# Optimization experiments

Measured on AMD Instinct MI355X. Metric: run time of the kernel, lower is better.

## Reference

```python
import jax, jax.numpy as jnp
import numpy as np

B, S, D, H = 32, 8192, 128, 256  # batch-of-MLPs, seq_len, emb_dim, hidden_dim
LN_EPS = 1e-5


def setup_inputs() -> dict:
    key = jax.random.key(0)
    k0, k1, k2, k3 = jax.random.split(key, 4)
    x = jax.random.normal(k0, (B, S, D), dtype=jnp.float32)
    # shared learned Q projection (torch Linear stores W as [out,in]; y = x @ W.T)
    Wq = jax.random.normal(k1, (D, D), dtype=jnp.float32) / np.float32(np.sqrt(D))
    # per-batch-index (non-shared) fast-weight MLP params
    W1 = jax.random.normal(k2, (B, D, H), dtype=jnp.float32) / np.float32(np.sqrt(D))
    b1 = jnp.zeros((B, H), dtype=jnp.float32)
    W2 = jax.random.normal(k3, (B, H, D), dtype=jnp.float32) / np.float32(np.sqrt(H))
    b2 = jnp.zeros((B, D), dtype=jnp.float32)
    gamma = jnp.ones((B, D), dtype=jnp.float32)
    beta = jnp.zeros((B, D), dtype=jnp.float32)
    return dict(x=x, Wq=Wq, W1=W1, b1=b1, W2=W2, b2=b2, gamma=gamma, beta=beta)


def reference(x, Wq, W1, b1, W2, b2, gamma, beta):
    # queries = silu(Q(x))
    q = jax.nn.silu(jnp.einsum('bsd,ed->bse', x, Wq))
    # torch F.normalize with default dim=1 -> L2-normalize over the sequence axis
    q = q / jnp.clip(jnp.linalg.norm(q, axis=1, keepdims=True), 1e-12)
    # ParallelMLPs: per-index MLP with distinct weights (grouped GEMM), + residual
    h = jax.nn.silu(jnp.einsum('bsd,bdh->bsh', q, W1) + b1[:, None, :])
    o = jnp.einsum('bsh,bhd->bsd', h, W2) + b2[:, None, :]
    mu = jnp.mean(o, axis=-1, keepdims=True)
    var = jnp.mean(jnp.square(o - mu), axis=-1, keepdims=True)
    ln = (o - mu) / jnp.sqrt(var + LN_EPS) * gamma[:, None, :] + beta[:, None, :]
    return ln + q
```

## Files before the change

### kernel.cpp

```cpp
#include <hip/hip_runtime.h>
#include <stdint.h>

#define B_ 32
#define S_ 8192
#define D_ 128
#define H_ 256

typedef __attribute__((ext_vector_type(4))) float f32x4;
typedef __attribute__((ext_vector_type(8))) short bf16x8;
typedef __attribute__((ext_vector_type(4))) unsigned int u32x4;

__device__ __forceinline__ unsigned short f2bf(float f) {
    union { float f; unsigned int u; } v; v.f = f;
    unsigned int r = v.u + 0x7fffu + ((v.u >> 16) & 1u);
    return (unsigned short)(r >> 16);
}
__device__ __forceinline__ float bf2f(unsigned short u) {
    union { unsigned int u; float f; } v; v.u = ((unsigned int)u) << 16;
    return v.f;
}
__device__ __forceinline__ float silu_f(float v) {
    return v / (1.0f + __expf(-v));
}
__device__ __forceinline__ unsigned int cvtpk(float lo, float hi) {
    unsigned int r;
    asm("v_cvt_pk_bf16_f32 %0, %1, %2" : "=v"(r) : "v"(lo), "v"(hi));
    return r;
}
__device__ __forceinline__ void gl16(const void* g, void* l) {
    __builtin_amdgcn_global_load_lds(
        (const __attribute__((address_space(1))) unsigned int*)g,
        (__attribute__((address_space(3))) unsigned int*)l, 16, 0, 0);
}

__global__ void k_prep(const float* __restrict__ Wq, const float* __restrict__ W1,
                       const float* __restrict__ W2,
                       unsigned short* __restrict__ wq_bf,
                       unsigned short* __restrict__ w1t,
                       unsigned short* __restrict__ w2s) {
    __shared__ __align__(16) unsigned short tile[64 * 64];
    int t = threadIdx.x, blk = blockIdx.x;
    if (blk < 512) {
        int b = blk >> 4, ht = (blk >> 2) & 3, dt = blk & 3;
        int h0 = ht * 64, d0 = dt * 32;
#pragma unroll
        for (int i = 0; i < 2; i++) {
            int idx = t + i * 256;
            int h = idx >> 3, d4 = (idx & 7) * 4;
            f32x4 v = *(const f32x4*)(W2 + ((size_t)(b * H_ + h0 + h)) * D_ + d0 + d4);
#pragma unroll
            for (int j = 0; j < 4; j++) tile[(d4 + j) * 64 + h] = f2bf(v[j]);
        }
        __syncthreads();
        int r = t >> 3, c = t & 7;
        int d = d0 + r;
        u32x4 v = *(const u32x4*)(tile + r * 64 + c * 8);
        *(u32x4*)((char*)w2s + (size_t)(b * 4 + ht) * 16384 + d * 128 + ((c ^ (d & 7)) << 4)) = v;
    } else if (blk < 768) {
        int a = blk - 512;
        int b = a >> 3, dt = (a >> 2) & 1, ht = a & 3;
        int d0 = dt * 64, h0 = ht * 64;
#pragma unroll
        for (int i = 0; i < 4; i++) {
            int idx = t + i * 256;
            int d = idx >> 4, h4 = (idx & 15) * 4;
            f32x4 v = *(const f32x4*)(W1 + ((size_t)(b * D_ + d0 + d)) * H_ + h0 + h4);
#pragma unroll
            for (int j = 0; j < 4; j++) tile[(h4 + j) * 64 + d] = f2bf(v[j]);
        }
        __syncthreads();
#pragma unroll
        for (int i = 0; i < 2; i++) {
            int idx = t + i * 256;
            int h = idx >> 3, c = idx & 7;
            u32x4 v = *(const u32x4*)(tile + h * 64 + c * 8);
            *(u32x4*)(w1t + ((size_t)(b * H_ + h0 + h)) * D_ + d0 + c * 8) = v;
        }
    } else {
        int i = (blk - 768) * 256 + t;
        wq_bf[i] = f2bf(Wq[i]);
    }
}

__global__ __launch_bounds__(256, 2) void k_qproj(
        const float* __restrict__ x, const unsigned short* __restrict__ wq_bf,
        unsigned short* __restrict__ q_ws, float* __restrict__ part) {
    __shared__ __align__(16) unsigned short lds_a[128 * 128];
    __shared__ __align__(16) unsigned short lds_b[128 * 128];
    __shared__ float lds_ss[4][128];

    int tid = threadIdx.x;
    int lane = tid & 63, w = tid >> 6;
    int g = lane >> 4, c15 = lane & 15;
    int blk = blockIdx.x;
    int b = blk >> 6, st = blk & 63;
    size_t rowbase = (size_t)b * S_ + (size_t)st * 128;
    const float* xg = x + rowbase * D_;

    char* pA = (char*)lds_a;
    char* pB = (char*)lds_b;

#pragma unroll
    for (int i = 0; i < 8; i++) {
        int idx = tid + i * 256;
        int row = idx >> 4, cb = idx & 15;
        u32x4 v = *(const u32x4*)(wq_bf + row * 128 + cb * 8);
        *(u32x4*)(pB + row * 256 + (((unsigned)cb ^ (unsigned)(row & 7)) << 4)) = v;
    }
#pragma unroll
    for (int i = 0; i < 16; i++) {
        int idx = tid + i * 256;
        int row = idx >> 5, c4 = idx & 31;
        f32x4 v = *(const f32x4*)(xg + (size_t)row * 128 + c4 * 4);
        union { unsigned short s[4]; unsigned long long u; } o;
        o.s[0] = f2bf(v[0]); o.s[1] = f2bf(v[1]); o.s[2] = f2bf(v[2]); o.s[3] = f2bf(v[3]);
        *(unsigned long long*)(pA + row * 256 + ((c4 * 8) ^ ((row & 7) << 4))) = o.u;
    }
    __syncthreads();

    f32x4 acc[2][8];
#pragma unroll
    for (int m = 0; m < 2; m++)
#pragma unroll
        for (int n = 0; n < 8; n++) acc[m][n] = (f32x4)0.0f;

#pragma unroll
    for (int kk = 0; kk < 4; kk++) {
        int kb = kk * 64 + (g << 4);
        bf16x8 a[2];
#pragma unroll
        for (int m = 0; m < 2; m++) {
            int row = (w << 5) + (m << 4) + c15;
            a[m] = *(const bf16x8*)(pA + row * 256 + (kb ^ ((row & 7) << 4)));
        }
#pragma unroll
        for (int n = 0; n < 8; n++) {
            int rowb = (n << 4) + c15;
            bf16x8 bb = *(const bf16x8*)(pB + rowb * 256 + (kb ^ ((rowb & 7) << 4)));
#pragma unroll
            for (int m = 0; m < 2; m++)
                acc[m][n] = __builtin_amdgcn_mfma_f32_16x16x32_bf16(a[m], bb, acc[m][n], 0, 0, 0);
        }
    }

    float ss[8];
#pragma unroll
    for (int n = 0; n < 8; n++) ss[n] = 0.0f;
#pragma unroll
    for (int m = 0; m < 2; m++)
#pragma unroll
        for (int n = 0; n < 8; n++)
#pragma unroll
            for (int r = 0; r < 4; r++) {
                float v = silu_f(acc[m][n][r]);
                acc[m][n][r] = v;
                ss[n] += v * v;
            }
#pragma unroll
    for (int n = 0; n < 8; n++) {
        float v = ss[n];
        v += __shfl_xor(v, 16, 64);
        v += __shfl_xor(v, 32, 64);
        if (lane < 16) lds_ss[w][(n << 4) + lane] = v;
    }
    __syncthreads();

#pragma unroll
    for (int m = 0; m < 2; m++)
#pragma unroll
        for (int n = 0; n < 8; n++)
#pragma unroll
            for (int r = 0; r < 4; r++) {
                int row = (w << 5) + (m << 4) + (g << 2) + r;
                int col = (n << 4) + c15;
                int byte = row * 256 + (((col >> 3) ^ (row & 7)) << 4) + ((col & 7) * 2);
                *(unsigned short*)(pA + byte) = f2bf(acc[m][n][r]);
            }
    __syncthreads();

    char* qimg = (char*)q_ws + (size_t)(b * 64 + st) * 32768;
#pragma unroll
    for (int i = 0; i < 8; i++) {
        int off = tid * 16 + i * 4096;
        *(u32x4*)(qimg + off) = *(const u32x4*)(pA + off);
    }
    if (tid < 128) {
        float s = lds_ss[0][tid] + lds_ss[1][tid] + lds_ss[2][tid] + lds_ss[3][tid];
        part[((size_t)b * 64 + st) * 128 + tid] = s;
    }
}

__global__ void k_scale(const float* __restrict__ part, float* __restrict__ scale) {
    int idx = blockIdx.x * 256 + threadIdx.x;
    int b = idx >> 7, e = idx & 127;
    const float* p = part + (size_t)b * 64 * 128 + e;
    float s = 0.0f;
    for (int t = 0; t < 64; t++) s += p[t * 128];
    scale[idx] = 1.0f / fmaxf(sqrtf(s), 1e-12f);
}

__global__ void k_wscale(unsigned short* __restrict__ w1t, const float* __restrict__ scale) {
    int blk = blockIdx.x;
    int b = blk >> 2;
    char* region = (char*)w1t + (size_t)blk * 16384;
    int t = threadIdx.x;
    u32x4 v[4]; int hh[4], cc[4];
#pragma unroll
    for (int i = 0; i < 4; i++) {
        int cid = t + i * 256;
        hh[i] = cid >> 4; cc[i] = cid & 15;
        v[i] = *(const u32x4*)(region + hh[i] * 256 + cc[i] * 16);
    }
    __syncthreads();
#pragma unroll
    for (int i = 0; i < 4; i++) {
        union { unsigned short s[8]; u32x4 u; } o;
        const unsigned short* pv = (const unsigned short*)&v[i];
        const float* sc = scale + b * D_ + cc[i] * 8;
#pragma unroll
        for (int j = 0; j < 8; j++) o.s[j] = f2bf(bf2f(pv[j]) * sc[j]);
        *(u32x4*)(region + hh[i] * 256 + ((cc[i] ^ (hh[i] & 7)) << 4)) = o.u;
    }
}

__global__ __launch_bounds__(256, 2) void k_mlp(
        const unsigned short* __restrict__ q_img, const float* __restrict__ scale,
        const unsigned short* __restrict__ w1s, const unsigned short* __restrict__ w2s,
        const float* __restrict__ b1, const float* __restrict__ b2,
        const float* __restrict__ gamma, const float* __restrict__ beta,
        float* __restrict__ out) {
    __shared__ __align__(16) char lds[81920];
    int tid = threadIdx.x;
    int lane = tid & 63, w = tid >> 6;
    int g = lane >> 4, c15 = lane & 15;
    int blk = blockIdx.x;
    int b = blk >> 6, st = blk & 63;

    const char* qimg = (const char*)q_img + (size_t)(b * 64 + st) * 32768;
    const char* w1img = (const char*)w1s + (size_t)(b * 4) * 16384;
    const char* w2img = (const char*)w2s + (size_t)(b * 4) * 16384;

#pragma unroll
    for (int i = 0; i < 8; i++) {
        int off = w * 1024 + i * 4096;
        gl16(qimg + off + lane * 16, lds + off);
    }
#pragma unroll
    for (int i = 0; i < 4; i++) {
        int off = w * 1024 + i * 4096;
        gl16(w1img + off + lane * 16, lds + 32768 + off);
        gl16(w2img + off + lane * 16, lds + 49152 + off);
    }
    __syncthreads();

    f32x4 acco[2][8];
#pragma unroll
    for (int sm = 0; sm < 2; sm++)
#pragma unroll
        for (int dn = 0; dn < 8; dn++) acco[sm][dn] = (f32x4)0.0f;

#pragma unroll 1
    for (int hc = 0; hc < 4; hc++) {
        f32x4 b1v[4];
#pragma unroll
        for (int n = 0; n < 4; n++)
            b1v[n] = *(const f32x4*)(b1 + b * H_ + hc * 64 + n * 16 + g * 4);

        f32x4 acch[2][4];
#pragma unroll
        for (int sm = 0; sm < 2; sm++)
#pragma unroll
            for (int n = 0; n < 4; n++) acch[sm][n] = (f32x4)0.0f;
#pragma unroll
        for (int kk = 0; kk < 4; kk++) {
            bf16x8 qf[2];
#pragma unroll
            for (int sm = 0; sm < 2; sm++) {
                int row = w * 32 + sm * 16 + c15;
                qf[sm] = *(const bf16x8*)(lds + row * 256 + (((kk * 4 + g) ^ (row & 7)) << 4));
            }
#pragma unroll
            for (int n = 0; n < 4; n++) {
                int row = n * 16 + c15;
                bf16x8 wf = *(const bf16x8*)(lds + 32768 + row * 256 + (((kk * 4 + g) ^ (row & 7)) << 4));
#pragma unroll
                for (int sm = 0; sm < 2; sm++)
                    acch[sm][n] = __builtin_amdgcn_mfma_f32_16x16x32_bf16(wf, qf[sm], acch[sm][n], 0, 0, 0);
            }
        }

#pragma unroll
        for (int sm = 0; sm < 2; sm++) {
            int rl = sm * 16 + c15;
#pragma unroll
            for (int n = 0; n < 4; n++) {
                float v0 = silu_f(acch[sm][n][0] + b1v[n][0]);
                float v1 = silu_f(acch[sm][n][1] + b1v[n][1]);
                float v2 = silu_f(acch[sm][n][2] + b1v[n][2]);
                float v3 = silu_f(acch[sm][n][3] + b1v[n][3]);
                unsigned int lo = cvtpk(v0, v1), hi = cvtpk(v2, v3);
                int byte = 65536 + w * 4096 + rl * 128 + ((n * 32 + g * 8) ^ ((rl & 7) << 4));
                *(unsigned long long*)(lds + byte) =
                    ((unsigned long long)hi << 32) | (unsigned long long)lo;
            }
        }

#pragma unroll
        for (int kt = 0; kt < 2; kt++) {
            bf16x8 ha[2];
#pragma unroll
            for (int sm = 0; sm < 2; sm++) {
                int rl = sm * 16 + c15;
                ha[sm] = *(const bf16x8*)(lds + 65536 + w * 4096 + rl * 128 +
                                          ((kt * 64 + g * 16) ^ ((rl & 7) << 4)));
            }
#pragma unroll
            for (int dn = 0; dn < 8; dn++) {
                int row = dn * 16 + c15;
                bf16x8 wf = *(const bf16x8*)(lds + 49152 + row * 128 + (((kt * 4 + g) ^ (row & 7)) << 4));
#pragma unroll
                for (int sm = 0; sm < 2; sm++)
                    acco[sm][dn] = __builtin_amdgcn_mfma_f32_16x16x32_bf16(ha[sm], wf, acco[sm][dn], 0, 0, 0);
            }
        }

        if (hc < 3) {
            __syncthreads();
#pragma unroll
            for (int i = 0; i < 4; i++) {
                int off = w * 1024 + i * 4096;
                gl16(w1img + (hc + 1) * 16384 + off + lane * 16, lds + 32768 + off);
                gl16(w2img + (hc + 1) * 16384 + off + lane * 16, lds + 49152 + off);
            }
            __syncthreads();
        }
    }

    float scv[8], gv[8], bev[8], b2v[8];
#pragma unroll
    for (int dn = 0; dn < 8; dn++) {
        int col = dn * 16 + c15;
        scv[dn] = scale[b * 128 + col];
        gv[dn] = gamma[b * 128 + col];
        bev[dn] = beta[b * 128 + col];
        b2v[dn] = b2[b * 128 + col];
    }
    float* og = out + ((size_t)b * S_ + (size_t)st * 128) * D_;
#pragma unroll
    for (int sm = 0; sm < 2; sm++) {
#pragma unroll
        for (int r = 0; r < 4; r++) {
            int row = w * 32 + sm * 16 + g * 4 + r;
            float v[8];
            float s = 0.0f, s2 = 0.0f;
#pragma unroll
            for (int dn = 0; dn < 8; dn++) {
                v[dn] = acco[sm][dn][r] + b2v[dn];
                s += v[dn]; s2 += v[dn] * v[dn];
            }
            s += __shfl_xor(s, 1, 64);  s2 += __shfl_xor(s2, 1, 64);
            s += __shfl_xor(s, 2, 64);  s2 += __shfl_xor(s2, 2, 64);
            s += __shfl_xor(s, 4, 64);  s2 += __shfl_xor(s2, 4, 64);
            s += __shfl_xor(s, 8, 64);  s2 += __shfl_xor(s2, 8, 64);
            float mu = s * (1.0f / 128.0f);
            float var = s2 * (1.0f / 128.0f) - mu * mu;
            float rstd = rsqrtf(var + 1e-5f);
#pragma unroll
            for (int dn = 0; dn < 8; dn++) {
                int col = dn * 16 + c15;
                int byte = row * 256 + (((col >> 3) ^ (row & 7)) << 4) + ((col & 7) * 2);
                float qv = bf2f(*(const unsigned short*)(lds + byte)) * scv[dn];
                og[(size_t)row * 128 + col] = (v[dn] - mu) * rstd * gv[dn] + bev[dn] + qv;
            }
        }
    }
}

extern "C" void kernel_launch(void* const* d_in, const int* in_sizes, int n_in,
                              void* d_out, int out_size, void* d_ws, size_t ws_size,
                              hipStream_t stream) {
    (void)in_sizes; (void)n_in; (void)out_size; (void)ws_size;
    const float* x     = (const float*)d_in[0];
    const float* Wq    = (const float*)d_in[1];
    const float* W1    = (const float*)d_in[2];
    const float* b1    = (const float*)d_in[3];
    const float* W2    = (const float*)d_in[4];
    const float* b2    = (const float*)d_in[5];
    const float* gamma = (const float*)d_in[6];
    const float* beta  = (const float*)d_in[7];
    float* out = (float*)d_out;

    char* ws = (char*)d_ws;
    unsigned short* wq_bf = (unsigned short*)(ws);
    unsigned short* w1t   = (unsigned short*)(ws + 32768);
    unsigned short* w2s   = (unsigned short*)(ws + 32768 + 2097152);
    float* part           = (float*)(ws + 32768 + 2 * 2097152);
    float* scale          = (float*)(ws + 32768 + 2 * 2097152 + 1048576);
    unsigned short* q_ws  = (unsigned short*)(ws + 32768 + 2 * 2097152 + 1048576 + 16384);

    hipLaunchKernelGGL(k_prep, dim3(832), dim3(256), 0, stream, Wq, W1, W2, wq_bf, w1t, w2s);
    hipLaunchKernelGGL(k_qproj, dim3(2048), dim3(256), 0, stream, x, wq_bf, q_ws, part);
    hipLaunchKernelGGL(k_scale, dim3(16), dim3(256), 0, stream, part, scale);
    hipLaunchKernelGGL(k_wscale, dim3(128), dim3(256), 0, stream, w1t, scale);
    hipLaunchKernelGGL(k_mlp, dim3(2048), dim3(256), 0, stream,
                       q_ws, scale, w1t, w2s, b1, b2, gamma, beta, out);
}
```

Before: 147.4 us.

## Switch MLP to 32x32x16 MFMA with register-resident hidden activations and double buffering

Rewrites the fused MLP kernel to use 32x32x16 bf16 MFMA tiles. Q fragments are held in registers, and the SiLU hidden activations are passed straight into the second GEMM via permlane32 swaps instead of a round trip through LDS. The weight, bias and q images are pre-laid out in MFMA fragment order, and the W1/W2 chunks are double-buffered so the next chunk loads while the current one computes, removing one barrier pair per chunk. The cost is more register pressure and a more intricate fragment layout that must match across the prep, qproj and mlp kernels.

```diff
diff --git a/kernel.cpp b/kernel.cpp
--- a/kernel.cpp
+++ b/kernel.cpp
@@ -7,6 +7,7 @@
 #define H_ 256
 
 typedef __attribute__((ext_vector_type(4))) float f32x4;
+typedef __attribute__((ext_vector_type(16))) float f32x16;
 typedef __attribute__((ext_vector_type(8))) short bf16x8;
 typedef __attribute__((ext_vector_type(4))) unsigned int u32x4;
 
@@ -27,6 +28,9 @@
     asm("v_cvt_pk_bf16_f32 %0, %1, %2" : "=v"(r) : "v"(lo), "v"(hi));
     return r;
 }
+__device__ __forceinline__ void plswap(unsigned int& a, unsigned int& b) {
+    asm("v_permlane32_swap_b32 %0, %1" : "+v"(a), "+v"(b));
+}
 __device__ __forceinline__ void gl16(const void* g, void* l) {
     __builtin_amdgcn_global_load_lds(
         (const __attribute__((address_space(1))) unsigned int*)g,
@@ -34,57 +38,67 @@
 }
 
 __global__ void k_prep(const float* __restrict__ Wq, const float* __restrict__ W1,
-                       const float* __restrict__ W2,
+                       const float* __restrict__ W2, const float* __restrict__ b1,
                        unsigned short* __restrict__ wq_bf,
-                       unsigned short* __restrict__ w1t,
-                       unsigned short* __restrict__ w2s) {
-    __shared__ __align__(16) unsigned short tile[64 * 64];
+                       unsigned short* __restrict__ w1s,
+                       unsigned short* __restrict__ w2s,
+                       float* __restrict__ b1r) {
+    __shared__ __align__(16) unsigned short tile[8192];
     int t = threadIdx.x, blk = blockIdx.x;
-    if (blk < 512) {
-        int b = blk >> 4, ht = (blk >> 2) & 3, dt = blk & 3;
-        int h0 = ht * 64, d0 = dt * 32;
-#pragma unroll
-        for (int i = 0; i < 2; i++) {
+    if (blk < 128) {
+        int b = blk >> 2, hc = blk & 3;
+#pragma unroll
+        for (int i = 0; i < 8; i++) {
             int idx = t + i * 256;
-            int h = idx >> 3, d4 = (idx & 7) * 4;
-            f32x4 v = *(const f32x4*)(W2 + ((size_t)(b * H_ + h0 + h)) * D_ + d0 + d4);
-#pragma unroll
-            for (int j = 0; j < 4; j++) tile[(d4 + j) * 64 + h] = f2bf(v[j]);
+            int d = idx >> 4, hj = idx & 15;
+            f32x4 v = *(const f32x4*)(W1 + ((size_t)(b * D_ + d)) * H_ + hc * 64 + hj * 4);
+#pragma unroll
+            for (int u = 0; u < 4; u++) tile[(hj * 4 + u) * 128 + d] = f2bf(v[u]);
         }
         __syncthreads();
-        int r = t >> 3, c = t & 7;
-        int d = d0 + r;
-        u32x4 v = *(const u32x4*)(tile + r * 64 + c * 8);
-        *(u32x4*)((char*)w2s + (size_t)(b * 4 + ht) * 16384 + d * 128 + ((c ^ (d & 7)) << 4)) = v;
-    } else if (blk < 768) {
-        int a = blk - 512;
-        int b = a >> 3, dt = (a >> 2) & 1, ht = a & 3;
-        int d0 = dt * 64, h0 = ht * 64;
+        char* img = (char*)w1s + (size_t)blk * 16384;
 #pragma unroll
         for (int i = 0; i < 4; i++) {
+            int c = t + i * 256;
+            int n = c >> 9, kk = (c >> 6) & 7, l = c & 63;
+            u32x4 v = *(const u32x4*)(tile + (n * 32 + (l & 31)) * 128 + kk * 16 + (l >> 5) * 8);
+            *(u32x4*)(img + c * 16) = v;
+        }
+    } else if (blk < 256) {
+        int a = blk - 128;
+        int b = a >> 2, hc = a & 3;
+#pragma unroll
+        for (int i = 0; i < 8; i++) {
             int idx = t + i * 256;
-            int d = idx >> 4, h4 = (idx & 15) * 4;
-            f32x4 v = *(const f32x4*)(W1 + ((size_t)(b * D_ + d0 + d)) * H_ + h0 + h4);
-#pragma unroll
-            for (int j = 0; j < 4; j++) tile[(h4 + j) * 64 + d] = f2bf(v[j]);
+            int h = idx >> 5, d4 = idx & 31;
+            f32x4 v = *(const f32x4*)(W2 + ((size_t)(b * H_ + hc * 64 + h)) * D_ + d4 * 4);
+#pragma unroll
+            for (int u = 0; u < 4; u++) tile[(d4 * 4 + u) * 64 + h] = f2bf(v[u]);
         }
         __syncthreads();
-#pragma unroll
-        for (int i = 0; i < 2; i++) {
-            int idx = t + i * 256;
-            int h = idx >> 3, c = idx & 7;
-            u32x4 v = *(const u32x4*)(tile + h * 64 + c * 8);
-            *(u32x4*)(w1t + ((size_t)(b * H_ + h0 + h)) * D_ + d0 + c * 8) = v;
-        }
+        char* img = (char*)w2s + (size_t)a * 16384;
+#pragma unroll
+        for (int i = 0; i < 4; i++) {
+            int c = t + i * 256;
+            int dn = c >> 8, n = (c >> 7) & 1, kk2 = (c >> 6) & 1, l = c & 63;
+            u32x4 v = *(const u32x4*)(tile + (dn * 32 + (l & 31)) * 64 + n * 32 + kk2 * 16 + (l >> 5) * 8);
+            *(u32x4*)(img + c * 16) = v;
+        }
+    } else if (blk < 320) {
+        int i = (blk - 256) * 256 + t;
+        wq_bf[i] = f2bf(Wq[i]);
     } else {
-        int i = (blk - 768) * 256 + t;
-        wq_bf[i] = f2bf(Wq[i]);
+        int idx = (blk - 320) * 256 + t;
+        int b = idx >> 8, rem = idx & 255;
+        int hc = rem >> 6, n = (rem >> 5) & 1, hi = (rem >> 4) & 1, r = rem & 15;
+        int h = hc * 64 + n * 32 + (r & 3) + 8 * (r >> 2) + 4 * hi;
+        b1r[idx] = b1[b * H_ + h];
     }
 }
 
 __global__ __launch_bounds__(256, 2) void k_qproj(
         const float* __restrict__ x, const unsigned short* __restrict__ wq_bf,
-        unsigned short* __restrict__ q_ws, float* __restrict__ part) {
+        unsigned short* __restrict__ q_img, float* __restrict__ part) {
     __shared__ __align__(16) unsigned short lds_a[128 * 128];
     __shared__ __align__(16) unsigned short lds_b[128 * 128];
     __shared__ float lds_ss[4][128];
@@ -112,9 +126,9 @@
         int idx = tid + i * 256;
         int row = idx >> 5, c4 = idx & 31;
         f32x4 v = *(const f32x4*)(xg + (size_t)row * 128 + c4 * 4);
-        union { unsigned short s[4]; unsigned long long u; } o;
-        o.s[0] = f2bf(v[0]); o.s[1] = f2bf(v[1]); o.s[2] = f2bf(v[2]); o.s[3] = f2bf(v[3]);
-        *(unsigned long long*)(pA + row * 256 + ((c4 * 8) ^ ((row & 7) << 4))) = o.u;
+        unsigned int lo = cvtpk(v[0], v[1]), hi2 = cvtpk(v[2], v[3]);
+        *(unsigned long long*)(pA + row * 256 + ((c4 * 8) ^ ((row & 7) << 4))) =
+            ((unsigned long long)hi2 << 32) | (unsigned long long)lo;
     }
     __syncthreads();
 
@@ -173,16 +187,17 @@
             for (int r = 0; r < 4; r++) {
                 int row = (w << 5) + (m << 4) + (g << 2) + r;
                 int col = (n << 4) + c15;
-                int byte = row * 256 + (((col >> 3) ^ (row & 7)) << 4) + ((col & 7) * 2);
+                int byte = (row >> 5) * 8192 + (col >> 4) * 1024 +
+                           ((row & 31) + ((col >> 3) & 1) * 32) * 16 + (col & 7) * 2;
                 *(unsigned short*)(pA + byte) = f2bf(acc[m][n][r]);
             }
     __syncthreads();
 
-    char* qimg = (char*)q_ws + (size_t)(b * 64 + st) * 32768;
+    char* qo = (char*)q_img + ((size_t)(b * 256 + st * 4)) * 8192;
 #pragma unroll
     for (int i = 0; i < 8; i++) {
         int off = tid * 16 + i * 4096;
-        *(u32x4*)(qimg + off) = *(const u32x4*)(pA + off);
+        *(u32x4*)(qo + off) = *(const u32x4*)(pA + off);
     }
     if (tid < 128) {
         float s = lds_ss[0][tid] + lds_ss[1][tid] + lds_ss[2][tid] + lds_ss[3][tid];
@@ -199,179 +214,147 @@
     scale[idx] = 1.0f / fmaxf(sqrtf(s), 1e-12f);
 }
 
-__global__ void k_wscale(unsigned short* __restrict__ w1t, const float* __restrict__ scale) {
+__global__ void k_wscale(unsigned short* __restrict__ w1s, const float* __restrict__ scale) {
     int blk = blockIdx.x;
     int b = blk >> 2;
-    char* region = (char*)w1t + (size_t)blk * 16384;
+    char* region = (char*)w1s + (size_t)blk * 16384;
     int t = threadIdx.x;
-    u32x4 v[4]; int hh[4], cc[4];
 #pragma unroll
     for (int i = 0; i < 4; i++) {
-        int cid = t + i * 256;
-        hh[i] = cid >> 4; cc[i] = cid & 15;
-        v[i] = *(const u32x4*)(region + hh[i] * 256 + cc[i] * 16);
-    }
-    __syncthreads();
-#pragma unroll
-    for (int i = 0; i < 4; i++) {
-        union { unsigned short s[8]; u32x4 u; } o;
-        const unsigned short* pv = (const unsigned short*)&v[i];
-        const float* sc = scale + b * D_ + cc[i] * 8;
-#pragma unroll
-        for (int j = 0; j < 8; j++) o.s[j] = f2bf(bf2f(pv[j]) * sc[j]);
-        *(u32x4*)(region + hh[i] * 256 + ((cc[i] ^ (hh[i] & 7)) << 4)) = o.u;
+        int c = t + i * 256;
+        int kk = (c >> 6) & 7, l = c & 63;
+        int d0 = kk * 16 + (l >> 5) * 8;
+        u32x4 v = *(const u32x4*)(region + c * 16);
+        const unsigned short* pv = (const unsigned short*)&v;
+        const float* sc = scale + b * D_ + d0;
+        u32x4 o;
+#pragma unroll
+        for (int j = 0; j < 4; j++)
+            o[j] = cvtpk(bf2f(pv[2 * j]) * sc[2 * j], bf2f(pv[2 * j + 1]) * sc[2 * j + 1]);
+        *(u32x4*)(region + c * 16) = o;
     }
 }
 
 __global__ __launch_bounds__(256, 2) void k_mlp(
         const unsigned short* __restrict__ q_img, const float* __restrict__ scale,
         const unsigned short* __restrict__ w1s, const unsigned short* __restrict__ w2s,
-        const float* __restrict__ b1, const float* __restrict__ b2,
+        const float* __restrict__ b1r, const float* __restrict__ b2,
         const float* __restrict__ gamma, const float* __restrict__ beta,
         float* __restrict__ out) {
-    __shared__ __align__(16) char lds[81920];
+    __shared__ __align__(16) char lds[65536];
     int tid = threadIdx.x;
     int lane = tid & 63, w = tid >> 6;
-    int g = lane >> 4, c15 = lane & 15;
+    int c31 = lane & 31, hi = lane >> 5;
     int blk = blockIdx.x;
     int b = blk >> 6, st = blk & 63;
 
-    const char* qimg = (const char*)q_img + (size_t)(b * 64 + st) * 32768;
-    const char* w1img = (const char*)w1s + (size_t)(b * 4) * 16384;
-    const char* w2img = (const char*)w2s + (size_t)(b * 4) * 16384;
-
-#pragma unroll
-    for (int i = 0; i < 8; i++) {
-        int off = w * 1024 + i * 4096;
-        gl16(qimg + off + lane * 16, lds + off);
-    }
-#pragma unroll
-    for (int i = 0; i < 4; i++) {
-        int off = w * 1024 + i * 4096;
-        gl16(w1img + off + lane * 16, lds + 32768 + off);
-        gl16(w2img + off + lane * 16, lds + 49152 + off);
-    }
+    const char* w1b = (const char*)w1s + (size_t)(b * 4) * 16384;
+    const char* w2b = (const char*)w2s + (size_t)(b * 4) * 16384;
+    size_t grp = (size_t)(b * 256 + st * 4 + w);
+    const char* qg = (const char*)q_img + grp * 8192;
+
+#define STAGE(bufoff, hcn) do {                                               \
+    _Pragma("unroll")                                                          \
+    for (int i_ = 0; i_ < 4; i_++) {                                           \
+        int off_ = w * 1024 + i_ * 4096;                                       \
+        gl16(w1b + (hcn) * 16384 + off_ + lane * 16, lds + (bufoff) + off_);   \
+        gl16(w2b + (hcn) * 16384 + off_ + lane * 16, lds + (bufoff) + 16384 + off_); \
+    } } while (0)
+
+    STAGE(0, 0);
+
+    bf16x8 qf[8];
+#pragma unroll
+    for (int kk = 0; kk < 8; kk++)
+        qf[kk] = *(const bf16x8*)(qg + kk * 1024 + lane * 16);
+
+    float scv[4], gv[4], bev[4];
+    f32x16 acco[4];
+#pragma unroll
+    for (int dn = 0; dn < 4; dn++) {
+        int d = dn * 32 + c31;
+        scv[dn] = scale[b * 128 + d];
+        gv[dn]  = gamma[b * 128 + d];
+        bev[dn] = beta[b * 128 + d];
+        float bb = b2[b * 128 + d];
+#pragma unroll
+        for (int e = 0; e < 16; e++) acco[dn][e] = bb;
+    }
+
     __syncthreads();
 
-    f32x4 acco[2][8];
-#pragma unroll
-    for (int sm = 0; sm < 2; sm++)
-#pragma unroll
-        for (int dn = 0; dn < 8; dn++) acco[sm][dn] = (f32x4)0.0f;
-
-#pragma unroll 1
+#pragma unroll
     for (int hc = 0; hc < 4; hc++) {
-        f32x4 b1v[4];
-#pragma unroll
-        for (int n = 0; n < 4; n++)
-            b1v[n] = *(const f32x4*)(b1 + b * H_ + hc * 64 + n * 16 + g * 4);
-
-        f32x4 acch[2][4];
-#pragma unroll
-        for (int sm = 0; sm < 2; sm++)
-#pragma unroll
-            for (int n = 0; n < 4; n++) acch[sm][n] = (f32x4)0.0f;
-#pragma unroll
-        for (int kk = 0; kk < 4; kk++) {
-            bf16x8 qf[2];
-#pragma unroll
-            for (int sm = 0; sm < 2; sm++) {
-                int row = w * 32 + sm * 16 + c15;
-                qf[sm] = *(const bf16x8*)(lds + row * 256 + (((kk * 4 + g) ^ (row & 7)) << 4));
+        int buf = (hc & 1) * 32768;
+        if (hc < 3) STAGE(buf ^ 32768, hc + 1);
+
+        bf16x8 pa[2][2];
+#pragma unroll
+        for (int n = 0; n < 2; n++) {
+            const float* b1p = b1r + ((b * 4 + hc) * 2 + n) * 32 + hi * 16;
+            f32x16 acch;
+#pragma unroll
+            for (int jq = 0; jq < 4; jq++) {
+                f32x4 bq = *(const f32x4*)(b1p + jq * 4);
+#pragma unroll
+                for (int e = 0; e < 4; e++) acch[jq * 4 + e] = bq[e];
             }
 #pragma unroll
-            for (int n = 0; n < 4; n++) {
-                int row = n * 16 + c15;
-                bf16x8 wf = *(const bf16x8*)(lds + 32768 + row * 256 + (((kk * 4 + g) ^ (row & 7)) << 4));
-#pragma unroll
-                for (int sm = 0; sm < 2; sm++)
-                    acch[sm][n] = __builtin_amdgcn_mfma_f32_16x16x32_bf16(wf, qf[sm], acch[sm][n], 0, 0, 0);
+            for (int kk = 0; kk < 8; kk++) {
+                bf16x8 wf = *(const bf16x8*)(lds + buf + n * 8192 + kk * 1024 + lane * 16);
+                acch = __builtin_amdgcn_mfma_f32_32x32x16_bf16(wf, qf[kk], acch, 0, 0, 0);
             }
-        }
-
-#pragma unroll
-        for (int sm = 0; sm < 2; sm++) {
-            int rl = sm * 16 + c15;
-#pragma unroll
-            for (int n = 0; n < 4; n++) {
-                float v0 = silu_f(acch[sm][n][0] + b1v[n][0]);
-                float v1 = silu_f(acch[sm][n][1] + b1v[n][1]);
-                float v2 = silu_f(acch[sm][n][2] + b1v[n][2]);
-                float v3 = silu_f(acch[sm][n][3] + b1v[n][3]);
-                unsigned int lo = cvtpk(v0, v1), hi = cvtpk(v2, v3);
-                int byte = 65536 + w * 4096 + rl * 128 + ((n * 32 + g * 8) ^ ((rl & 7) << 4));
-                *(unsigned long long*)(lds + byte) =
-                    ((unsigned long long)hi << 32) | (unsigned long long)lo;
-            }
-        }
-
-#pragma unroll
-        for (int kt = 0; kt < 2; kt++) {
-            bf16x8 ha[2];
-#pragma unroll
-            for (int sm = 0; sm < 2; sm++) {
-                int rl = sm * 16 + c15;
-                ha[sm] = *(const bf16x8*)(lds + 65536 + w * 4096 + rl * 128 +
-                                          ((kt * 64 + g * 16) ^ ((rl & 7) << 4)));
-            }
-#pragma unroll
-            for (int dn = 0; dn < 8; dn++) {
-                int row = dn * 16 + c15;
-                bf16x8 wf = *(const bf16x8*)(lds + 49152 + row * 128 + (((kt * 4 + g) ^ (row & 7)) << 4));
-#pragma unroll
-                for (int sm = 0; sm < 2; sm++)
-                    acco[sm][dn] = __builtin_amdgcn_mfma_f32_16x16x32_bf16(ha[sm], wf, acco[sm][dn], 0, 0, 0);
-            }
-        }
-
-        if (hc < 3) {
-            __syncthreads();
-#pragma unroll
-            for (int i = 0; i < 4; i++) {
-                int off = w * 1024 + i * 4096;
-                gl16(w1img + (hc + 1) * 16384 + off + lane * 16, lds + 32768 + off);
-                gl16(w2img + (hc + 1) * 16384 + off + lane * 16, lds + 49152 + off);
-            }
-            __syncthreads();
-        }
-    }
-
-    float scv[8], gv[8], bev[8], b2v[8];
-#pragma unroll
-    for (int dn = 0; dn < 8; dn++) {
-        int col = dn * 16 + c15;
-        scv[dn] = scale[b * 128 + col];
-        gv[dn] = gamma[b * 128 + col];
-        bev[dn] = beta[b * 128 + col];
-        b2v[dn] = b2[b * 128 + col];
-    }
-    float* og = out + ((size_t)b * S_ + (size_t)st * 128) * D_;
-#pragma unroll
-    for (int sm = 0; sm < 2; sm++) {
-#pragma unroll
-        for (int r = 0; r < 4; r++) {
-            int row = w * 32 + sm * 16 + g * 4 + r;
-            float v[8];
-            float s = 0.0f, s2 = 0.0f;
-#pragma unroll
-            for (int dn = 0; dn < 8; dn++) {
-                v[dn] = acco[sm][dn][r] + b2v[dn];
-                s += v[dn]; s2 += v[dn] * v[dn];
-            }
-            s += __shfl_xor(s, 1, 64);  s2 += __shfl_xor(s2, 1, 64);
-            s += __shfl_xor(s, 2, 64);  s2 += __shfl_xor(s2, 2, 64);
-            s += __shfl_xor(s, 4, 64);  s2 += __shfl_xor(s2, 4, 64);
-            s += __shfl_xor(s, 8, 64);  s2 += __shfl_xor(s2, 8, 64);
-            float mu = s * (1.0f / 128.0f);
-            float var = s2 * (1.0f / 128.0f) - mu * mu;
-            float rstd = rsqrtf(var + 1e-5f);
-#pragma unroll
-            for (int dn = 0; dn < 8; dn++) {
-                int col = dn * 16 + c15;
-                int byte = row * 256 + (((col >> 3) ^ (row & 7)) << 4) + ((col & 7) * 2);
-                float qv = bf2f(*(const unsigned short*)(lds + byte)) * scv[dn];
-                og[(size_t)row * 128 + col] = (v[dn] - mu) * rstd * gv[dn] + bev[dn] + qv;
-            }
+            float sv[16];
+#pragma unroll
+            for (int r = 0; r < 16; r++) sv[r] = silu_f(acch[r]);
+            unsigned int P[8];
+#pragma unroll
+            for (int p = 0; p < 8; p++) P[p] = cvtpk(sv[2 * p], sv[2 * p + 1]);
+            plswap(P[0], P[2]); plswap(P[1], P[3]);
+            plswap(P[4], P[6]); plswap(P[5], P[7]);
+            union { unsigned int u[4]; bf16x8 v; } f0, f1;
+            f0.u[0] = P[0]; f0.u[1] = P[1]; f0.u[2] = P[2]; f0.u[3] = P[3];
+            f1.u[0] = P[4]; f1.u[1] = P[5]; f1.u[2] = P[6]; f1.u[3] = P[7];
+            pa[n][0] = f0.v; pa[n][1] = f1.v;
+        }
+
+#pragma unroll
+        for (int dn = 0; dn < 4; dn++)
+#pragma unroll
+            for (int n = 0; n < 2; n++)
+#pragma unroll
+                for (int kk2 = 0; kk2 < 2; kk2++) {
+                    bf16x8 wf2 = *(const bf16x8*)(lds + buf + 16384 + dn * 4096 +
+                                                  n * 2048 + kk2 * 1024 + lane * 16);
+                    acco[dn] = __builtin_amdgcn_mfma_f32_32x32x16_bf16(pa[n][kk2], wf2, acco[dn], 0, 0, 0);
+                }
+
+        if (hc < 3) __syncthreads();
+    }
+#undef STAGE
+
+    int lane_off = (c31 >> 4) * 1024 + ((c31 >> 3) & 1) * 512 + (c31 & 7) * 2 + hi * 64;
+    float* og = out + grp * 32 * 128;
+#pragma unroll
+    for (int r = 0; r < 16; r++) {
+        float v0 = acco[0][r], v1 = acco[1][r], v2 = acco[2][r], v3 = acco[3][r];
+        float s1 = (v0 + v1) + (v2 + v3);
+        float s2 = (v0 * v0 + v1 * v1) + (v2 * v2 + v3 * v3);
+        s1 += __shfl_xor(s1, 1, 64);   s2 += __shfl_xor(s2, 1, 64);
+        s1 += __shfl_xor(s1, 2, 64);   s2 += __shfl_xor(s2, 2, 64);
+        s1 += __shfl_xor(s1, 4, 64);   s2 += __shfl_xor(s2, 4, 64);
+        s1 += __shfl_xor(s1, 8, 64);   s2 += __shfl_xor(s2, 8, 64);
+        s1 += __shfl_xor(s1, 16, 64);  s2 += __shfl_xor(s2, 16, 64);
+        float mu = s1 * (1.0f / 128.0f);
+        float var = s2 * (1.0f / 128.0f) - mu * mu;
+        float rstd = rsqrtf(var + 1e-5f);
+        int srow0 = (r & 3) + 8 * (r >> 2);
+        int row = srow0 + 4 * hi;
+#pragma unroll
+        for (int dn = 0; dn < 4; dn++) {
+            float qv = bf2f(*(const unsigned short*)(qg + dn * 2048 + srow0 * 16 + lane_off)) * scv[dn];
+            float o = (acco[dn][r] - mu) * rstd * gv[dn] + bev[dn] + qv;
+            og[(size_t)row * 128 + dn * 32 + c31] = o;
         }
     }
 }
@@ -392,16 +375,17 @@
 
     char* ws = (char*)d_ws;
     unsigned short* wq_bf = (unsigned short*)(ws);
-    unsigned short* w1t   = (unsigned short*)(ws + 32768);
-    unsigned short* w2s   = (unsigned short*)(ws + 32768 + 2097152);
-    float* part           = (float*)(ws + 32768 + 2 * 2097152);
-    float* scale          = (float*)(ws + 32768 + 2 * 2097152 + 1048576);
-    unsigned short* q_ws  = (unsigned short*)(ws + 32768 + 2 * 2097152 + 1048576 + 16384);
-
-    hipLaunchKernelGGL(k_prep, dim3(832), dim3(256), 0, stream, Wq, W1, W2, wq_bf, w1t, w2s);
-    hipLaunchKernelGGL(k_qproj, dim3(2048), dim3(256), 0, stream, x, wq_bf, q_ws, part);
+    unsigned short* w1s   = (unsigned short*)(ws + 32768);
+    unsigned short* w2s   = (unsigned short*)(ws + 2129920);
+    float* part           = (float*)(ws + 4227072);
+    float* scale          = (float*)(ws + 5275648);
+    float* b1r            = (float*)(ws + 5292032);
+    unsigned short* q_img = (unsigned short*)(ws + 5324800);
+
+    hipLaunchKernelGGL(k_prep, dim3(352), dim3(256), 0, stream, Wq, W1, W2, b1, wq_bf, w1s, w2s, b1r);
+    hipLaunchKernelGGL(k_qproj, dim3(2048), dim3(256), 0, stream, x, wq_bf, q_img, part);
     hipLaunchKernelGGL(k_scale, dim3(16), dim3(256), 0, stream, part, scale);
-    hipLaunchKernelGGL(k_wscale, dim3(128), dim3(256), 0, stream, w1t, scale);
+    hipLaunchKernelGGL(k_wscale, dim3(128), dim3(256), 0, stream, w1s, scale);
     hipLaunchKernelGGL(k_mlp, dim3(2048), dim3(256), 0, stream,
-                       q_ws, scale, w1t, w2s, b1, b2, gamma, beta, out);
-}
+                       q_img, scale, w1s, w2s, b1r, b2, gamma, beta, out);
+}
```

Measured after the change: 152.2 us. +3.3%, slower.
